# Optimization experiments

Measured on AMD Instinct MI355X. Metric: run time of the kernel, lower is better.

Reference implementation:

```python
import jax, jax.numpy as jnp
import numpy as np

BM = 64; BN = 64          # block_m, block_n
NKM = BM // 4; NKN = BN // 4   # tokens sampled per block (16)
# topk_newtype bands: cumulative-pooled-attention fraction -> granularity value (0 = skip block)
RATIO_BANDS = [(1, 0.05), (2, 0.15), (4, 0.25), (8, 0.5)]


def setup_inputs() -> dict:
    key = jax.random.key(0)
    kq, kk, kv, ki, kj = jax.random.split(key, 5)
    B, H, L, D = 1, 8, 4096, 64
    q = jax.random.normal(kq, (B, H, L, D), jnp.float32)
    k = jax.random.normal(kk, (B, H, L, D), jnp.float32)
    v = jax.random.normal(kv, (B, H, L, D), jnp.float32)
    # distinct in-block sample positions, shared across blocks per (B,H)
    # (mirrors torch.topk(torch.rand(B,H,1,block), sample_num))
    sample_idx_q = jnp.argsort(jax.random.uniform(ki, (B, H, BM)), axis=-1)[..., :NKM].astype(jnp.int32)
    sample_idx_k = jnp.argsort(jax.random.uniform(kj, (B, H, BN)), axis=-1)[..., :NKN].astype(jnp.int32)
    return {"q": q, "k": k, "v": v, "sample_idx_q": sample_idx_q, "sample_idx_k": sample_idx_k}


def _sample_blocks(x, idx, bs, nk):
    # x: [B,H,L,D]; idx: [B,H,nk] in-block positions -> [B,H,nb*nk,D]
    B, H, L, D = x.shape
    nb = L // bs
    xb = x.reshape(B, H, nb, bs, D)
    gidx = jnp.broadcast_to(idx[:, :, None, :, None], (B, H, nb, nk, D))
    return jnp.take_along_axis(xb, gidx, axis=3).reshape(B, H, nb * nk, D)


def _block_mask(q, k, sample_idx_q, sample_idx_k):
    # pooled downsampled attention -> per-(q_block,k_block) keep mask (topk_newtype)
    B, H, L, D = q.shape
    qb, kb = L // BM, L // BN
    sq = _sample_blocks(q, sample_idx_q, BM, NKM)  # [B,H,qb*NKM,D]
    sk = _sample_blocks(k, sample_idx_k, BN, NKN)  # [B,H,kb*NKN,D]
    scores = jnp.einsum('bhqd,bhkd->bhqk', sq, sk) / jnp.sqrt(jnp.float32(D))
    attn = jax.nn.softmax(scores, axis=-1)
    # NKM x NKN sum-pooling == block-level pooled attention mass  [B,H,qb,kb]
    pooling = attn.reshape(B, H, qb, NKM, kb, NKN).sum(axis=(3, 5))
    # rank key-blocks per q-block row by pooled mass, band by cumulative fraction
    order = jnp.argsort(-pooling, axis=-1)
    sp = jnp.take_along_axis(pooling, order, axis=-1)
    cs = jnp.cumsum(sp, axis=-1)
    frac_before = (cs - sp) / cs[..., -1:]
    val = jnp.zeros_like(sp)
    for g, hi in RATIO_BANDS[::-1]:
        val = jnp.where(frac_before < hi, jnp.float32(g), val)
    rank = jnp.argsort(order, axis=-1)          # inverse permutation
    mask_vals = jnp.take_along_axis(val, rank, axis=-1)  # [B,H,qb,kb] in {0,1,2,4,8}
    return mask_vals > 0


def reference(q, k, v, sample_idx_q, sample_idx_k):
    B, H, L, D = q.shape
    attend = _block_mask(q, k, sample_idx_q, sample_idx_k)            # [B,H,qb,kb]
    attend_tok = jnp.repeat(jnp.repeat(attend, BM, axis=2), BN, axis=3)  # [B,H,L,L]
    scores = jnp.einsum('bhqd,bhkd->bhqk', q, k) / jnp.sqrt(jnp.float32(D))
    scores = jnp.where(attend_tok, scores, jnp.float32(-1e30))
    p = jax.nn.softmax(scores, axis=-1)
    return jnp.einsum('bhqk,bhkd->bhqd', p, v)
```

## Files before the change

### kernel.cpp

```cpp
#include <hip/hip_runtime.h>
#include <hip/hip_bf16.h>

#define H_ 8
#define L_ 4096
#define D_ 64
#define NB_ 64

typedef __attribute__((ext_vector_type(8))) short bf16x8;
typedef __attribute__((ext_vector_type(4))) float f32x4;

__device__ __forceinline__ unsigned short f2bf(float x) {
    unsigned u = __float_as_uint(x);
    u += 0x7fff + ((u >> 16) & 1);
    return (unsigned short)(u >> 16);
}
__device__ __forceinline__ float bf2f(unsigned short s) {
    return __uint_as_float(((unsigned)s) << 16);
}

__global__ __launch_bounds__(256) void prep_kernel(
    const float* __restrict__ q, const float* __restrict__ k, const float* __restrict__ v,
    const int* __restrict__ sidxk,
    unsigned short* __restrict__ qhi, unsigned short* __restrict__ qlo,
    unsigned short* __restrict__ khi,
    unsigned short* __restrict__ vth,
    unsigned short* __restrict__ skh, unsigned short* __restrict__ skl)
{
    const int h  = blockIdx.x >> 6;
    const int tb = blockIdx.x & 63;
    const int tid = threadIdx.x;
    __shared__ float vst[64][68];

    const size_t te = ((size_t)(h*64 + tb)) << 12;
    const float4* qg = (const float4*)(q + te);
    for (int i4 = tid; i4 < 1024; i4 += 256) {
        float4 t = qg[i4];
        ushort4 hi, lo;
        hi.x = f2bf(t.x); lo.x = f2bf(t.x - bf2f(hi.x));
        hi.y = f2bf(t.y); lo.y = f2bf(t.y - bf2f(hi.y));
        hi.z = f2bf(t.z); lo.z = f2bf(t.z - bf2f(hi.z));
        hi.w = f2bf(t.w); lo.w = f2bf(t.w - bf2f(hi.w));
        *(ushort4*)(qhi + te + i4*4) = hi;
        *(ushort4*)(qlo + te + i4*4) = lo;
    }
    const float4* kg = (const float4*)(k + te);
    for (int i4 = tid; i4 < 1024; i4 += 256) {
        float4 t = kg[i4];
        int r = i4 >> 4, c4 = i4 & 15;
        int sch = (c4 >> 1) ^ ((r >> 2) & 7);
        ushort4 hi;
        hi.x = f2bf(t.x); hi.y = f2bf(t.y); hi.z = f2bf(t.z); hi.w = f2bf(t.w);
        *(ushort4*)(khi + te + r*64 + sch*8 + (c4 & 1)*4) = hi;
    }
    {
        int t = tid >> 4, d4 = tid & 15;
        int srow = tb*64 + sidxk[h*16 + t];
        float4 x = *(const float4*)(k + ((size_t)h*L_ + srow)*D_ + d4*4);
        ushort4 hi, lo;
        hi.x = f2bf(x.x); lo.x = f2bf(x.x - bf2f(hi.x));
        hi.y = f2bf(x.y); lo.y = f2bf(x.y - bf2f(hi.y));
        hi.z = f2bf(x.z); lo.z = f2bf(x.z - bf2f(hi.z));
        hi.w = f2bf(x.w); lo.w = f2bf(x.w - bf2f(hi.w));
        int sch = (d4 >> 1) ^ (t & 7);
        size_t dst = ((size_t)h*1024 + tb*16 + t)*64 + sch*8 + (d4 & 1)*4;
        *(ushort4*)(skh + dst) = hi;
        *(ushort4*)(skl + dst) = lo;
    }
    const float4* vg = (const float4*)(v + te);
    for (int i4 = tid; i4 < 1024; i4 += 256) {
        float4 t = vg[i4];
        *(float4*)&vst[i4 >> 4][(i4 & 15)*4] = t;
    }
    __syncthreads();
    for (int u = tid; u < 512; u += 256) {
        int d = u >> 3, kc8 = u & 7;
        int sch = kc8 ^ (d & 7);
        ushort4 h0, h1;
        h0.x = f2bf(vst[kc8*8+0][d]); h0.y = f2bf(vst[kc8*8+1][d]);
        h0.z = f2bf(vst[kc8*8+2][d]); h0.w = f2bf(vst[kc8*8+3][d]);
        h1.x = f2bf(vst[kc8*8+4][d]); h1.y = f2bf(vst[kc8*8+5][d]);
        h1.z = f2bf(vst[kc8*8+6][d]); h1.w = f2bf(vst[kc8*8+7][d]);
        *(ushort4*)(vth + te + d*64 + sch*8 + 0) = h0;
        *(ushort4*)(vth + te + d*64 + sch*8 + 4) = h1;
    }
}

__global__ __launch_bounds__(256, 4) void mask_mfma(
    const unsigned short* __restrict__ qhi, const unsigned short* __restrict__ qlo,
    const unsigned short* __restrict__ skh, const unsigned short* __restrict__ skl,
    const int* __restrict__ sidxq,
    unsigned long long* __restrict__ maskbits)
{
    const int h    = blockIdx.x & 7;
    const int qb   = blockIdx.x >> 3;
    const int tid  = threadIdx.x;
    const int wave = tid >> 6;
    const int lane = tid & 63;
    const int l16  = lane & 15;
    const int quad = lane >> 4;

    __shared__ __align__(16) unsigned short ch[8192];
    __shared__ __align__(16) unsigned short cl[8192];
    __shared__ float E[16][64];
    __shared__ float Z[16];
    __shared__ float pooled[64];

    for (int e = tid; e < 16*64; e += 256) (&E[0][0])[e] = 0.f;

    const int iqr = sidxq[h*16 + l16];
    const size_t qo = (((size_t)(h*64 + qb)) << 12) + (size_t)iqr*64;
    bf16x8 qh[2], ql[2];
    qh[0] = *(const bf16x8*)(qhi + qo + quad*8);
    qh[1] = *(const bf16x8*)(qhi + qo + 32 + quad*8);
    ql[0] = *(const bf16x8*)(qlo + qo + quad*8);
    ql[1] = *(const bf16x8*)(qlo + qo + 32 + quad*8);
    __syncthreads();

    for (int cc = 0; cc < 8; ++cc) {
        const bf16x8* gh = (const bf16x8*)(skh + ((size_t)h*1024 + cc*128)*64);
        const bf16x8* gl = (const bf16x8*)(skl + ((size_t)h*1024 + cc*128)*64);
        for (int i = tid; i < 1024; i += 256) {
            ((bf16x8*)ch)[i] = gh[i];
            ((bf16x8*)cl)[i] = gl[i];
        }
        __syncthreads();

        #pragma unroll
        for (int tt = 0; tt < 2; ++tt) {
            const int kb = cc*8 + wave*2 + tt;
            const int nb = (wave*2 + tt)*16;
            f32x4 sacc = (f32x4){0.f, 0.f, 0.f, 0.f};
            #pragma unroll
            for (int kc = 0; kc < 2; ++kc) {
                const int off = (nb + l16)*64 + (((kc*4 + quad) ^ (l16 & 7))*8);
                bf16x8 kh = *(const bf16x8*)&ch[off];
                bf16x8 kl = *(const bf16x8*)&cl[off];
                sacc = __builtin_amdgcn_mfma_f32_16x16x32_bf16(qh[kc], kh, sacc, 0, 0, 0);
                sacc = __builtin_amdgcn_mfma_f32_16x16x32_bf16(qh[kc], kl, sacc, 0, 0, 0);
                sacc = __builtin_amdgcn_mfma_f32_16x16x32_bf16(ql[kc], kh, sacc, 0, 0, 0);
                sacc = __builtin_amdgcn_mfma_f32_16x16x32_bf16(ql[kc], kl, sacc, 0, 0, 0);
            }
            #pragma unroll
            for (int r = 0; r < 4; ++r) {
                float p = __expf(sacc[r] * 0.125f);
                p += __shfl_xor(p, 1);
                p += __shfl_xor(p, 2);
                p += __shfl_xor(p, 4);
                p += __shfl_xor(p, 8);
                if (l16 == 0) E[quad*4 + r][kb] = p;
            }
        }
        __syncthreads();
    }

    if (tid < 16) {
        float s = 0.f;
        #pragma unroll
        for (int kb = 0; kb < 64; ++kb) s += E[tid][kb];
        Z[tid] = s;
    }
    __syncthreads();
    if (tid < 64) {
        float s = 0.f;
        #pragma unroll
        for (int t = 0; t < 16; ++t) s += E[t][tid] / Z[t];
        pooled[tid] = s;
    }
    __syncthreads();
    if (tid < 64) {
        float pi = pooled[tid];
        float tot = 0.f, bef = 0.f;
        for (int j2 = 0; j2 < 64; ++j2) {
            float pj = pooled[j2];
            tot += pj;
            if (pj > pi || (pj == pi && j2 < tid)) bef += pj;
        }
        bool att = (bef / tot) < 0.5f;
        unsigned long long bits = __ballot(att);
        if (tid == 0) maskbits[h*64 + qb] = bits;
    }
}

__global__ __launch_bounds__(256, 2) void attn_wave(
    const unsigned short* __restrict__ qhi,
    const unsigned short* __restrict__ khi,
    const unsigned short* __restrict__ vth,
    const unsigned long long* __restrict__ maskbits,
    float* __restrict__ out)
{
    const int h    = blockIdx.x & 7;
    const int qb   = blockIdx.x >> 3;
    const int tid  = threadIdx.x;
    const int wave = tid >> 6;
    const int lane = tid & 63;
    const int l16  = lane & 15;
    const int quad = lane >> 4;

    __shared__ __align__(16) char SM[66560];
    unsigned short* Qh = (unsigned short*)SM;
    unsigned short* ps = (unsigned short*)(SM + 9216 + wave*11264);

    const size_t qbase = ((size_t)(h*64 + qb)) << 12;

    for (int c = tid; c < 512; c += 256) {
        int row = c >> 3, cc = c & 7;
        int sw = cc ^ ((row >> 2) & 7);
        uint4 th = *(const uint4*)(qhi + qbase + row*64 + cc*8);
        *(uint4*)&Qh[row*72 + sw*8] = th;
    }

    unsigned long long rem = maskbits[(h << 6) + qb];
    for (int s = 0; s < wave; ++s) rem &= rem - 1;
    int cur = rem ? (int)__builtin_ctzll(rem) : -1;

    const bf16x8 ones = {0x3F80, 0x3F80, 0x3F80, 0x3F80, 0x3F80, 0x3F80, 0x3F80, 0x3F80};

    f32x4 lacc[4];
    f32x4 oacc[4][4];
    #pragma unroll
    for (int qt = 0; qt < 4; ++qt) {
        lacc[qt] = (f32x4){0.f, 0.f, 0.f, 0.f};
        #pragma unroll
        for (int dt = 0; dt < 4; ++dt) oacc[qt][dt] = (f32x4){0.f, 0.f, 0.f, 0.f};
    }

    bf16x8 kf[4][2], vf[4][2];
    if (cur >= 0) {
        const size_t tb = ((size_t)(h*64 + cur)) << 12;
        #pragma unroll
        for (int t = 0; t < 4; ++t)
            #pragma unroll
            for (int kc = 0; kc < 2; ++kc) {
                kf[t][kc] = *(const bf16x8*)(khi + tb + (l16*4 + t)*64 + (((kc*4 + quad) ^ (l16 & 7))*8));
                vf[t][kc] = *(const bf16x8*)(vth + tb + (t*16 + l16)*64 + (((kc*4 + quad) ^ (l16 & 7))*8));
            }
    }
    __syncthreads();

    while (cur >= 0) {
        rem &= rem - 1; rem &= rem - 1; rem &= rem - 1; rem &= rem - 1;
        const int nxt = rem ? (int)__builtin_ctzll(rem) : -1;

        #pragma unroll
        for (int qt = 0; qt < 4; ++qt) {
            const int xb = (qt*4 + (l16 >> 2)) & 7;
            bf16x8 ah[2];
            #pragma unroll
            for (int kc = 0; kc < 2; ++kc) {
                const int off = (qt*16 + l16)*72 + (((kc*4 + quad) ^ xb)*8);
                ah[kc] = *(const bf16x8*)&Qh[off];
            }
            f32x4 sacc[4];
            #pragma unroll
            for (int t = 0; t < 4; ++t) sacc[t] = (f32x4){0.f, 0.f, 0.f, 0.f};
            __builtin_amdgcn_s_setprio(1);
            #pragma unroll
            for (int t = 0; t < 4; ++t)
                #pragma unroll
                for (int kc = 0; kc < 2; ++kc)
                    sacc[t] = __builtin_amdgcn_mfma_f32_16x16x32_bf16(ah[kc], kf[t][kc], sacc[t], 0, 0, 0);
            __builtin_amdgcn_s_setprio(0);
            #pragma unroll
            for (int r = 0; r < 4; ++r) {
                float p0 = __builtin_amdgcn_exp2f(fmaf(sacc[0][r], 0.18033688f, -23.083121f));
                float p1 = __builtin_amdgcn_exp2f(fmaf(sacc[1][r], 0.18033688f, -23.083121f));
                float p2 = __builtin_amdgcn_exp2f(fmaf(sacc[2][r], 0.18033688f, -23.083121f));
                float p3 = __builtin_amdgcn_exp2f(fmaf(sacc[3][r], 0.18033688f, -23.083121f));
                __hip_bfloat162 a01 = __float22bfloat162_rn(make_float2(p0, p1));
                __hip_bfloat162 a23 = __float22bfloat162_rn(make_float2(p2, p3));
                uint2 w; w.x = *(unsigned*)&a01; w.y = *(unsigned*)&a23;
                *(uint2*)&ps[(qt*16 + quad*4 + r)*88 + l16*4] = w;
            }
        }
        if (nxt >= 0) {
            const size_t tb = ((size_t)(h*64 + nxt)) << 12;
            #pragma unroll
            for (int t = 0; t < 4; ++t)
                #pragma unroll
                for (int kc = 0; kc < 2; ++kc)
                    kf[t][kc] = *(const bf16x8*)(khi + tb + (l16*4 + t)*64 + (((kc*4 + quad) ^ (l16 & 7))*8));
        }
        #pragma unroll
        for (int qt = 0; qt < 4; ++qt) {
            bf16x8 pf0 = *(const bf16x8*)&ps[(qt*16 + l16)*88 + quad*8];
            bf16x8 pf1 = *(const bf16x8*)&ps[(qt*16 + l16)*88 + 32 + quad*8];
            __builtin_amdgcn_s_setprio(1);
            lacc[qt] = __builtin_amdgcn_mfma_f32_16x16x32_bf16(pf0, ones, lacc[qt], 0, 0, 0);
            lacc[qt] = __builtin_amdgcn_mfma_f32_16x16x32_bf16(pf1, ones, lacc[qt], 0, 0, 0);
            #pragma unroll
            for (int dt = 0; dt < 4; ++dt) {
                oacc[qt][dt] = __builtin_amdgcn_mfma_f32_16x16x32_bf16(pf0, vf[dt][0], oacc[qt][dt], 0, 0, 0);
                oacc[qt][dt] = __builtin_amdgcn_mfma_f32_16x16x32_bf16(pf1, vf[dt][1], oacc[qt][dt], 0, 0, 0);
            }
            __builtin_amdgcn_s_setprio(0);
        }
        if (nxt >= 0) {
            const size_t tb = ((size_t)(h*64 + nxt)) << 12;
            #pragma unroll
            for (int dt = 0; dt < 4; ++dt)
                #pragma unroll
                for (int kc = 0; kc < 2; ++kc)
                    vf[dt][kc] = *(const bf16x8*)(vth + tb + (dt*16 + l16)*64 + (((kc*4 + quad) ^ (l16 & 7))*8));
        }
        cur = nxt;
    }

    __syncthreads();
    float* ored = (float*)SM;
    float* lred = (float*)(SM + 65536);
    #pragma unroll
    for (int qt = 0; qt < 4; ++qt) {
        #pragma unroll
        for (int dt = 0; dt < 4; ++dt)
            #pragma unroll
            for (int r = 0; r < 4; ++r)
                ored[wave*4096 + (qt*16 + quad*4 + r)*64 + dt*16 + l16] = oacc[qt][dt][r];
        if (l16 == 0) {
            #pragma unroll
            for (int r = 0; r < 4; ++r)
                lred[wave*64 + qt*16 + quad*4 + r] = lacc[qt][r];
        }
    }
    __syncthreads();
    {
        const int row = tid >> 2;
        const int d0  = (tid & 3) << 4;
        float l = lred[row] + lred[64 + row] + lred[128 + row] + lred[192 + row];
        float inv = 1.f / l;
        float* og = out + ((size_t)h*L_ + (size_t)qb*64 + row)*D_ + d0;
        #pragma unroll
        for (int j = 0; j < 16; j += 4) {
            float4 a = *(float4*)&ored[0*4096 + row*64 + d0 + j];
            float4 b = *(float4*)&ored[1*4096 + row*64 + d0 + j];
            float4 c = *(float4*)&ored[2*4096 + row*64 + d0 + j];
            float4 d = *(float4*)&ored[3*4096 + row*64 + d0 + j];
            float4 rr;
            rr.x = (a.x + b.x + c.x + d.x) * inv;
            rr.y = (a.y + b.y + c.y + d.y) * inv;
            rr.z = (a.z + b.z + c.z + d.z) * inv;
            rr.w = (a.w + b.w + c.w + d.w) * inv;
            *(float4*)(og + j) = rr;
        }
    }
}

__global__ __launch_bounds__(256, 4) void mask_kernel4(
    const float* __restrict__ q, const float* __restrict__ k,
    const int* __restrict__ sidxq, const int* __restrict__ sidxk,
    unsigned long long* __restrict__ maskbits)
{
    const int h   = blockIdx.x >> 6;
    const int qb  = blockIdx.x & 63;
    const int tid = threadIdx.x;
    const int rg  = tid >> 5;
    const int cg  = tid & 31;

    __shared__ float sq[16][68];
    __shared__ float skc[128][68];
    __shared__ float E[16][64];
    __shared__ float Z[16];
    __shared__ float pooled[64];
    __shared__ int iq[16], ik[16];

    if (tid < 16) { iq[tid] = sidxq[h*16 + tid]; ik[tid] = sidxk[h*16 + tid]; }
    for (int e = tid; e < 16*64; e += 256) (&E[0][0])[e] = 0.f;
    __syncthreads();
    {
        int j = tid >> 4, d4 = tid & 15;
        int grow = h*L_ + qb*64 + iq[j];
        *(float4*)&sq[j][d4*4] = *(const float4*)(q + (size_t)grow*D_ + d4*4);
    }
    for (int cc = 0; cc < 8; ++cc) {
        for (int i = tid; i < 2048; i += 256) {
            int col = i >> 4, d4 = i & 15;
            int colg = cc*128 + col;
            int grow = h*L_ + (colg >> 4)*64 + ik[colg & 15];
            *(float4*)&skc[col][d4*4] = *(const float4*)(k + (size_t)grow*D_ + d4*4);
        }
        __syncthreads();
        float acc[2][4] = {{0.f,0.f,0.f,0.f},{0.f,0.f,0.f,0.f}};
        #pragma unroll 4
        for (int d4 = 0; d4 < 16; ++d4) {
            float4 qv0 = *(const float4*)&sq[rg*2 + 0][d4*4];
            float4 qv1 = *(const float4*)&sq[rg*2 + 1][d4*4];
            #pragma unroll
            for (int j = 0; j < 4; ++j) {
                float4 kv = *(const float4*)&skc[cg + 32*j][d4*4];
                acc[0][j] += qv0.x*kv.x + qv0.y*kv.y + qv0.z*kv.z + qv0.w*kv.w;
                acc[1][j] += qv1.x*kv.x + qv1.y*kv.y + qv1.z*kv.z + qv1.w*kv.w;
            }
        }
        #pragma unroll
        for (int j = 0; j < 4; ++j) {
            int kb = cc*8 + (cg >> 4) + 2*j;
            #pragma unroll
            for (int i = 0; i < 2; ++i) {
                float p = __expf(acc[i][j] * 0.125f);
                p += __shfl_xor(p, 1);
                p += __shfl_xor(p, 2);
                p += __shfl_xor(p, 4);
                p += __shfl_xor(p, 8);
                if ((cg & 15) == 0) E[rg*2 + i][kb] += p;
            }
        }
        __syncthreads();
    }
    if (tid < 16) {
        float s = 0.f;
        #pragma unroll
        for (int kb = 0; kb < 64; ++kb) s += E[tid][kb];
        Z[tid] = s;
    }
    __syncthreads();
    if (tid < 64) {
        float s = 0.f;
        #pragma unroll
        for (int t = 0; t < 16; ++t) s += E[t][tid] / Z[t];
        pooled[tid] = s;
    }
    __syncthreads();
    if (tid < 64) {
        float pi = pooled[tid];
        float tot = 0.f, bef = 0.f;
        for (int j2 = 0; j2 < 64; ++j2) {
            float pj = pooled[j2];
            tot += pj;
            if (pj > pi || (pj == pi && j2 < tid)) bef += pj;
        }
        bool att = (bef / tot) < 0.5f;
        unsigned long long bits = __ballot(att);
        if (tid == 0) maskbits[h*64 + qb] = bits;
    }
}

__global__ __launch_bounds__(256, 3) void attn_v3(
    const float* __restrict__ q, const float* __restrict__ k, const float* __restrict__ v,
    const unsigned long long* __restrict__ maskbits, float* __restrict__ out)
{
    const int h = blockIdx.x >> 6, qb = blockIdx.x & 63;
    const int tid = threadIdx.x, wave = tid >> 6, lane = tid & 63;
    const int l16 = lane & 15, quad = lane >> 4;
    __shared__ __align__(16) unsigned short ks_hi[64][72];
    __shared__ __align__(16) unsigned short ks_lo[64][72];
    __shared__ __align__(16) unsigned short vt_hi[64][72];
    __shared__ __align__(16) unsigned short vt_lo[64][72];
    __shared__ __align__(16) unsigned short ps[4][16][72];

    const float4* qg = (const float4*)(q + ((size_t)h*L_ + (size_t)qb*64)*D_);
    for (int i4 = tid; i4 < 1024; i4 += 256) {
        float4 t = qg[i4];
        int r = i4 >> 4, c = (i4 & 15) << 2;
        ushort4 hi, lo;
        hi.x = f2bf(t.x); lo.x = f2bf(t.x - bf2f(hi.x));
        hi.y = f2bf(t.y); lo.y = f2bf(t.y - bf2f(hi.y));
        hi.z = f2bf(t.z); lo.z = f2bf(t.z - bf2f(hi.z));
        hi.w = f2bf(t.w); lo.w = f2bf(t.w - bf2f(hi.w));
        *(ushort4*)&ks_hi[r][c] = hi;
        *(ushort4*)&ks_lo[r][c] = lo;
    }
    const unsigned long long bm = maskbits[(h << 6) + qb];
    __syncthreads();
    bf16x8 qhi2[2], qlo2[2];
    #pragma unroll
    for (int kc = 0; kc < 2; ++kc) {
        qhi2[kc] = *(const bf16x8*)&ks_hi[wave*16 + l16][kc*32 + quad*8];
        qlo2[kc] = *(const bf16x8*)&ks_lo[wave*16 + l16][kc*32 + quad*8];
    }
    __syncthreads();
    float m_i[4], l_i[4];
    f32x4 oacc[4];
    #pragma unroll
    for (int r = 0; r < 4; ++r) { m_i[r] = -1e30f; l_i[r] = 0.f; }
    #pragma unroll
    for (int t = 0; t < 4; ++t) oacc[t] = (f32x4){0.f, 0.f, 0.f, 0.f};
    for (int kb = 0; kb < 64; ++kb) {
        if (!((bm >> kb) & 1ull)) continue;
        const float4* kg = (const float4*)(k + ((size_t)h*L_ + (size_t)kb*64)*D_);
        const float*  vg = v + ((size_t)h*L_ + (size_t)kb*64)*D_;
        for (int i4 = tid; i4 < 1024; i4 += 256) {
            float4 t = kg[i4];
            int r = i4 >> 4, c = (i4 & 15) << 2;
            ushort4 hi, lo;
            hi.x = f2bf(t.x); lo.x = f2bf(t.x - bf2f(hi.x));
            hi.y = f2bf(t.y); lo.y = f2bf(t.y - bf2f(hi.y));
            hi.z = f2bf(t.z); lo.z = f2bf(t.z - bf2f(hi.z));
            hi.w = f2bf(t.w); lo.w = f2bf(t.w - bf2f(hi.w));
            *(ushort4*)&ks_hi[r][c] = hi;
            *(ushort4*)&ks_lo[r][c] = lo;
        }
        for (int tsk = tid; tsk < 512; tsk += 256) {
            int rp = tsk >> 4;
            int c  = (tsk & 15) << 2;
            float4 a0 = *(const float4*)(vg + (size_t)(2*rp)*D_ + c);
            float4 a1 = *(const float4*)(vg + (size_t)(2*rp+1)*D_ + c);
            #pragma unroll
            for (int j = 0; j < 4; ++j) {
                float x0 = (j==0)?a0.x:(j==1)?a0.y:(j==2)?a0.z:a0.w;
                float x1 = (j==0)?a1.x:(j==1)?a1.y:(j==2)?a1.z:a1.w;
                unsigned short h0 = f2bf(x0), h1b = f2bf(x1);
                *(unsigned*)&vt_hi[c+j][2*rp] = (unsigned)h0 | ((unsigned)h1b << 16);
                unsigned short lo0 = f2bf(x0 - bf2f(h0)), lo1 = f2bf(x1 - bf2f(h1b));
                *(unsigned*)&vt_lo[c+j][2*rp] = (unsigned)lo0 | ((unsigned)lo1 << 16);
            }
        }
        __syncthreads();
        f32x4 sacc[4];
        #pragma unroll
        for (int t = 0; t < 4; ++t) sacc[t] = (f32x4){0.f, 0.f, 0.f, 0.f};
        #pragma unroll
        for (int t = 0; t < 4; ++t) {
            #pragma unroll
            for (int kc = 0; kc < 2; ++kc) {
                bf16x8 khi2 = *(const bf16x8*)&ks_hi[t*16 + l16][kc*32 + quad*8];
                bf16x8 klo2 = *(const bf16x8*)&ks_lo[t*16 + l16][kc*32 + quad*8];
                sacc[t] = __builtin_amdgcn_mfma_f32_16x16x32_bf16(qhi2[kc], khi2, sacc[t], 0, 0, 0);
                sacc[t] = __builtin_amdgcn_mfma_f32_16x16x32_bf16(qhi2[kc], klo2, sacc[t], 0, 0, 0);
                sacc[t] = __builtin_amdgcn_mfma_f32_16x16x32_bf16(qlo2[kc], khi2, sacc[t], 0, 0, 0);
            }
        }
        #pragma unroll
        for (int t = 0; t < 4; ++t) sacc[t] *= 0.125f;
        float rowmax[4];
        #pragma unroll
        for (int r = 0; r < 4; ++r)
            rowmax[r] = fmaxf(fmaxf(sacc[0][r], sacc[1][r]), fmaxf(sacc[2][r], sacc[3][r]));
        #pragma unroll
        for (int off = 1; off < 16; off <<= 1)
            #pragma unroll
            for (int r = 0; r < 4; ++r)
                rowmax[r] = fmaxf(rowmax[r], __shfl_xor(rowmax[r], off));
        float al[4], rs[4];
        #pragma unroll
        for (int r = 0; r < 4; ++r) {
            float mnew = fmaxf(m_i[r], rowmax[r]);
            al[r] = __expf(m_i[r] - mnew);
            m_i[r] = mnew;
            float acc = 0.f;
            #pragma unroll
            for (int t = 0; t < 4; ++t) {
                float p = __expf(sacc[t][r] - mnew);
                unsigned short pb = f2bf(p);
                ps[wave][quad*4 + r][t*16 + l16] = pb;
                acc += bf2f(pb);
            }
            rs[r] = acc;
        }
        #pragma unroll
        for (int off = 1; off < 16; off <<= 1)
            #pragma unroll
            for (int r = 0; r < 4; ++r)
                rs[r] += __shfl_xor(rs[r], off);
        #pragma unroll
        for (int r = 0; r < 4; ++r) l_i[r] = l_i[r] * al[r] + rs[r];
        #pragma unroll
        for (int t = 0; t < 4; ++t)
            #pragma unroll
            for (int r = 0; r < 4; ++r) oacc[t][r] *= al[r];
        bf16x8 pf[2];
        #pragma unroll
        for (int kc = 0; kc < 2; ++kc)
            pf[kc] = *(const bf16x8*)&ps[wave][l16][kc*32 + quad*8];
        #pragma unroll
        for (int t = 0; t < 4; ++t) {
            #pragma unroll
            for (int kc = 0; kc < 2; ++kc) {
                bf16x8 vhif = *(const bf16x8*)&vt_hi[t*16 + l16][kc*32 + quad*8];
                bf16x8 vlof = *(const bf16x8*)&vt_lo[t*16 + l16][kc*32 + quad*8];
                oacc[t] = __builtin_amdgcn_mfma_f32_16x16x32_bf16(pf[kc], vhif, oacc[t], 0, 0, 0);
                oacc[t] = __builtin_amdgcn_mfma_f32_16x16x32_bf16(pf[kc], vlof, oacc[t], 0, 0, 0);
            }
        }
        __syncthreads();
    }
    float* og = out + ((size_t)h*L_ + (size_t)qb*64)*D_ + (size_t)(wave*16 + quad*4)*D_;
    #pragma unroll
    for (int r = 0; r < 4; ++r) {
        float inv = 1.f / l_i[r];
        #pragma unroll
        for (int t = 0; t < 4; ++t)
            og[(size_t)r*D_ + t*16 + l16] = oacc[t][r] * inv;
    }
}

extern "C" void kernel_launch(void* const* d_in, const int* in_sizes, int n_in,
                              void* d_out, int out_size, void* d_ws, size_t ws_size,
                              hipStream_t stream) {
    const float* q = (const float*)d_in[0];
    const float* k = (const float*)d_in[1];
    const float* v = (const float*)d_in[2];
    const int* siq = (const int*)d_in[3];
    const int* sik = (const int*)d_in[4];
    float* out = (float*)d_out;

    char* ws = (char*)d_ws;
    unsigned long long* mask = (unsigned long long*)ws;
    const size_t TEN = (size_t)H_*L_*D_;
    const size_t SKN = (size_t)H_*1024*64;
    unsigned short* qhi = (unsigned short*)(ws + 4096);
    unsigned short* qlo = qhi + TEN;
    unsigned short* khi = qlo + TEN;
    unsigned short* vth = khi + TEN;
    unsigned short* skh = vth + TEN;
    unsigned short* skl = skh + SKN;
    const size_t need = 4096 + (4*TEN + 2*SKN)*sizeof(unsigned short);

    if (ws_size >= need) {
        prep_kernel<<<dim3(H_*NB_), dim3(256), 0, stream>>>(q, k, v, sik, qhi, qlo, khi, vth, skh, skl);
        mask_mfma<<<dim3(H_*NB_), dim3(256), 0, stream>>>(qhi, qlo, skh, skl, siq, mask);
        attn_wave<<<dim3(H_*NB_), dim3(256), 0, stream>>>(qhi, khi, vth, mask, out);
    } else {
        mask_kernel4<<<dim3(H_*NB_), dim3(256), 0, stream>>>(q, k, siq, sik, mask);
        attn_v3<<<dim3(H_*NB_), dim3(256), 0, stream>>>(q, k, v, mask, out);
    }
}
```

Measured before the change: 134.7 us.

## Fuse block-mask computation into attention kernel and drop MFMA priority hints

Merges the mask kernel into the attention kernel: each workgroup first computes its q-block's pooled sampled attention and keep-bitmask in shared memory (reusing the attention kernel's LDS buffer), then runs sparse attention directly from that bitmask. This removes one kernel launch and the global round-trip of the mask. The mask phase now runs at the attention kernel's occupancy bound (2 instead of 4) and is serialized before attention within each block. Separately, the s_setprio raises around the MFMA sections are removed.

```diff
diff --git a/kernel.cpp b/kernel.cpp
--- a/kernel.cpp
+++ b/kernel.cpp
@@ -85,107 +85,12 @@
     }
 }
 
-__global__ __launch_bounds__(256, 4) void mask_mfma(
+__global__ __launch_bounds__(256, 2) void mask_attn(
     const unsigned short* __restrict__ qhi, const unsigned short* __restrict__ qlo,
+    const unsigned short* __restrict__ khi,
+    const unsigned short* __restrict__ vth,
     const unsigned short* __restrict__ skh, const unsigned short* __restrict__ skl,
     const int* __restrict__ sidxq,
-    unsigned long long* __restrict__ maskbits)
-{
-    const int h    = blockIdx.x & 7;
-    const int qb   = blockIdx.x >> 3;
-    const int tid  = threadIdx.x;
-    const int wave = tid >> 6;
-    const int lane = tid & 63;
-    const int l16  = lane & 15;
-    const int quad = lane >> 4;
-
-    __shared__ __align__(16) unsigned short ch[8192];
-    __shared__ __align__(16) unsigned short cl[8192];
-    __shared__ float E[16][64];
-    __shared__ float Z[16];
-    __shared__ float pooled[64];
-
-    for (int e = tid; e < 16*64; e += 256) (&E[0][0])[e] = 0.f;
-
-    const int iqr = sidxq[h*16 + l16];
-    const size_t qo = (((size_t)(h*64 + qb)) << 12) + (size_t)iqr*64;
-    bf16x8 qh[2], ql[2];
-    qh[0] = *(const bf16x8*)(qhi + qo + quad*8);
-    qh[1] = *(const bf16x8*)(qhi + qo + 32 + quad*8);
-    ql[0] = *(const bf16x8*)(qlo + qo + quad*8);
-    ql[1] = *(const bf16x8*)(qlo + qo + 32 + quad*8);
-    __syncthreads();
-
-    for (int cc = 0; cc < 8; ++cc) {
-        const bf16x8* gh = (const bf16x8*)(skh + ((size_t)h*1024 + cc*128)*64);
-        const bf16x8* gl = (const bf16x8*)(skl + ((size_t)h*1024 + cc*128)*64);
-        for (int i = tid; i < 1024; i += 256) {
-            ((bf16x8*)ch)[i] = gh[i];
-            ((bf16x8*)cl)[i] = gl[i];
-        }
-        __syncthreads();
-
-        #pragma unroll
-        for (int tt = 0; tt < 2; ++tt) {
-            const int kb = cc*8 + wave*2 + tt;
-            const int nb = (wave*2 + tt)*16;
-            f32x4 sacc = (f32x4){0.f, 0.f, 0.f, 0.f};
-            #pragma unroll
-            for (int kc = 0; kc < 2; ++kc) {
-                const int off = (nb + l16)*64 + (((kc*4 + quad) ^ (l16 & 7))*8);
-                bf16x8 kh = *(const bf16x8*)&ch[off];
-                bf16x8 kl = *(const bf16x8*)&cl[off];
-                sacc = __builtin_amdgcn_mfma_f32_16x16x32_bf16(qh[kc], kh, sacc, 0, 0, 0);
-                sacc = __builtin_amdgcn_mfma_f32_16x16x32_bf16(qh[kc], kl, sacc, 0, 0, 0);
-                sacc = __builtin_amdgcn_mfma_f32_16x16x32_bf16(ql[kc], kh, sacc, 0, 0, 0);
-                sacc = __builtin_amdgcn_mfma_f32_16x16x32_bf16(ql[kc], kl, sacc, 0, 0, 0);
-            }
-            #pragma unroll
-            for (int r = 0; r < 4; ++r) {
-                float p = __expf(sacc[r] * 0.125f);
-                p += __shfl_xor(p, 1);
-                p += __shfl_xor(p, 2);
-                p += __shfl_xor(p, 4);
-                p += __shfl_xor(p, 8);
-                if (l16 == 0) E[quad*4 + r][kb] = p;
-            }
-        }
-        __syncthreads();
-    }
-
-    if (tid < 16) {
-        float s = 0.f;
-        #pragma unroll
-        for (int kb = 0; kb < 64; ++kb) s += E[tid][kb];
-        Z[tid] = s;
-    }
-    __syncthreads();
-    if (tid < 64) {
-        float s = 0.f;
-        #pragma unroll
-        for (int t = 0; t < 16; ++t) s += E[t][tid] / Z[t];
-        pooled[tid] = s;
-    }
-    __syncthreads();
-    if (tid < 64) {
-        float pi = pooled[tid];
-        float tot = 0.f, bef = 0.f;
-        for (int j2 = 0; j2 < 64; ++j2) {
-            float pj = pooled[j2];
-            tot += pj;
-            if (pj > pi || (pj == pi && j2 < tid)) bef += pj;
-        }
-        bool att = (bef / tot) < 0.5f;
-        unsigned long long bits = __ballot(att);
-        if (tid == 0) maskbits[h*64 + qb] = bits;
-    }
-}
-
-__global__ __launch_bounds__(256, 2) void attn_wave(
-    const unsigned short* __restrict__ qhi,
-    const unsigned short* __restrict__ khi,
-    const unsigned short* __restrict__ vth,
-    const unsigned long long* __restrict__ maskbits,
     float* __restrict__ out)
 {
     const int h    = blockIdx.x & 7;
@@ -197,10 +102,97 @@
     const int quad = lane >> 4;
 
     __shared__ __align__(16) char SM[66560];
+    __shared__ unsigned long long bmShared;
+
+    const size_t qbase = (((size_t)(h*64 + qb)) << 12);
+
+    {
+        unsigned short* ch = (unsigned short*)SM;
+        unsigned short* cl = (unsigned short*)(SM + 16384);
+        float* E  = (float*)(SM + 32768);
+        float* Zz = (float*)(SM + 36864);
+        float* pooled = (float*)(SM + 36928);
+
+        for (int e = tid; e < 16*64; e += 256) E[e] = 0.f;
+
+        const int iqr = sidxq[h*16 + l16];
+        const size_t qo = qbase + (size_t)iqr*64;
+        bf16x8 qh[2], ql[2];
+        qh[0] = *(const bf16x8*)(qhi + qo + quad*8);
+        qh[1] = *(const bf16x8*)(qhi + qo + 32 + quad*8);
+        ql[0] = *(const bf16x8*)(qlo + qo + quad*8);
+        ql[1] = *(const bf16x8*)(qlo + qo + 32 + quad*8);
+        __syncthreads();
+
+        for (int cc = 0; cc < 8; ++cc) {
+            const bf16x8* gh = (const bf16x8*)(skh + ((size_t)h*1024 + cc*128)*64);
+            const bf16x8* gl = (const bf16x8*)(skl + ((size_t)h*1024 + cc*128)*64);
+            for (int i = tid; i < 1024; i += 256) {
+                ((bf16x8*)ch)[i] = gh[i];
+                ((bf16x8*)cl)[i] = gl[i];
+            }
+            __syncthreads();
+
+            #pragma unroll
+            for (int tt = 0; tt < 2; ++tt) {
+                const int kb = cc*8 + wave*2 + tt;
+                const int nb = (wave*2 + tt)*16;
+                f32x4 sacc = (f32x4){0.f, 0.f, 0.f, 0.f};
+                #pragma unroll
+                for (int kc = 0; kc < 2; ++kc) {
+                    const int off = (nb + l16)*64 + (((kc*4 + quad) ^ (l16 & 7))*8);
+                    bf16x8 kh = *(const bf16x8*)&ch[off];
+                    bf16x8 kl = *(const bf16x8*)&cl[off];
+                    sacc = __builtin_amdgcn_mfma_f32_16x16x32_bf16(qh[kc], kh, sacc, 0, 0, 0);
+                    sacc = __builtin_amdgcn_mfma_f32_16x16x32_bf16(qh[kc], kl, sacc, 0, 0, 0);
+                    sacc = __builtin_amdgcn_mfma_f32_16x16x32_bf16(ql[kc], kh, sacc, 0, 0, 0);
+                    sacc = __builtin_amdgcn_mfma_f32_16x16x32_bf16(ql[kc], kl, sacc, 0, 0, 0);
+                }
+                #pragma unroll
+                for (int r = 0; r < 4; ++r) {
+                    float p = __expf(sacc[r] * 0.125f);
+                    p += __shfl_xor(p, 1);
+                    p += __shfl_xor(p, 2);
+                    p += __shfl_xor(p, 4);
+                    p += __shfl_xor(p, 8);
+                    if (l16 == 0) E[(quad*4 + r)*64 + kb] = p;
+                }
+            }
+            __syncthreads();
+        }
+
+        if (tid < 16) {
+            float s = 0.f;
+            #pragma unroll
+            for (int kb = 0; kb < 64; ++kb) s += E[tid*64 + kb];
+            Zz[tid] = s;
+        }
+        __syncthreads();
+        if (tid < 64) {
+            float s = 0.f;
+            #pragma unroll
+            for (int t = 0; t < 16; ++t) s += E[t*64 + tid] / Zz[t];
+            pooled[tid] = s;
+        }
+        __syncthreads();
+        if (tid < 64) {
+            float pi = pooled[tid];
+            float tot = 0.f, bef = 0.f;
+            for (int j2 = 0; j2 < 64; ++j2) {
+                float pj = pooled[j2];
+                tot += pj;
+                if (pj > pi || (pj == pi && j2 < tid)) bef += pj;
+            }
+            bool att = (bef / tot) < 0.5f;
+            unsigned long long bits = __ballot(att);
+            if (tid == 0) bmShared = bits;
+        }
+        __syncthreads();
+    }
+    const unsigned long long bm = bmShared;
+
     unsigned short* Qh = (unsigned short*)SM;
     unsigned short* ps = (unsigned short*)(SM + 9216 + wave*11264);
-
-    const size_t qbase = ((size_t)(h*64 + qb)) << 12;
 
     for (int c = tid; c < 512; c += 256) {
         int row = c >> 3, cc = c & 7;
@@ -209,7 +201,7 @@
         *(uint4*)&Qh[row*72 + sw*8] = th;
     }
 
-    unsigned long long rem = maskbits[(h << 6) + qb];
+    unsigned long long rem = bm;
     for (int s = 0; s < wave; ++s) rem &= rem - 1;
     int cur = rem ? (int)__builtin_ctzll(rem) : -1;
 
@@ -253,13 +245,11 @@
             f32x4 sacc[4];
             #pragma unroll
             for (int t = 0; t < 4; ++t) sacc[t] = (f32x4){0.f, 0.f, 0.f, 0.f};
-            __builtin_amdgcn_s_setprio(1);
             #pragma unroll
             for (int t = 0; t < 4; ++t)
                 #pragma unroll
                 for (int kc = 0; kc < 2; ++kc)
                     sacc[t] = __builtin_amdgcn_mfma_f32_16x16x32_bf16(ah[kc], kf[t][kc], sacc[t], 0, 0, 0);
-            __builtin_amdgcn_s_setprio(0);
             #pragma unroll
             for (int r = 0; r < 4; ++r) {
                 float p0 = __builtin_amdgcn_exp2f(fmaf(sacc[0][r], 0.18033688f, -23.083121f));
@@ -284,7 +274,6 @@
         for (int qt = 0; qt < 4; ++qt) {
             bf16x8 pf0 = *(const bf16x8*)&ps[(qt*16 + l16)*88 + quad*8];
             bf16x8 pf1 = *(const bf16x8*)&ps[(qt*16 + l16)*88 + 32 + quad*8];
-            __builtin_amdgcn_s_setprio(1);
             lacc[qt] = __builtin_amdgcn_mfma_f32_16x16x32_bf16(pf0, ones, lacc[qt], 0, 0, 0);
             lacc[qt] = __builtin_amdgcn_mfma_f32_16x16x32_bf16(pf1, ones, lacc[qt], 0, 0, 0);
             #pragma unroll
@@ -292,7 +281,6 @@
                 oacc[qt][dt] = __builtin_amdgcn_mfma_f32_16x16x32_bf16(pf0, vf[dt][0], oacc[qt][dt], 0, 0, 0);
                 oacc[qt][dt] = __builtin_amdgcn_mfma_f32_16x16x32_bf16(pf1, vf[dt][1], oacc[qt][dt], 0, 0, 0);
             }
-            __builtin_amdgcn_s_setprio(0);
         }
         if (nxt >= 0) {
             const size_t tb = ((size_t)(h*64 + nxt)) << 12;
@@ -606,8 +594,7 @@
 
     if (ws_size >= need) {
         prep_kernel<<<dim3(H_*NB_), dim3(256), 0, stream>>>(q, k, v, sik, qhi, qlo, khi, vth, skh, skl);
-        mask_mfma<<<dim3(H_*NB_), dim3(256), 0, stream>>>(qhi, qlo, skh, skl, siq, mask);
-        attn_wave<<<dim3(H_*NB_), dim3(256), 0, stream>>>(qhi, khi, vth, mask, out);
+        mask_attn<<<dim3(H_*NB_), dim3(256), 0, stream>>>(qhi, qlo, khi, vth, skh, skl, siq, out);
     } else {
         mask_kernel4<<<dim3(H_*NB_), dim3(256), 0, stream>>>(q, k, siq, sik, mask);
         attn_v3<<<dim3(H_*NB_), dim3(256), 0, stream>>>(q, k, v, mask, out);
```

Result: faster. 129.7 us (-3.7%).
